# Kernel optimization log

Hardware: AMD Instinct MI355X
Metric: run time of the kernel (lower is better)

The kernel has to match this reference:

```python
import jax, jax.numpy as jnp
import numpy as np

B, N, K, LEN_INIT = 4, 4096, 10, 3
LEN_INPUT = 3 * (K + 1) + 3 * K + LEN_INIT  # 66


def setup_inputs() -> dict:
    key = jax.random.key(0)
    ks = jax.random.split(key, 6)
    return {
        "position": jax.random.normal(ks[0], (B, N, 3), dtype=jnp.float32),
        "velocity": jax.random.normal(ks[1], (B, N, 3), dtype=jnp.float32),
        "init_config": jax.random.normal(ks[2], (B, LEN_INIT), dtype=jnp.float32),
        "W1": jax.random.normal(ks[3], (32, LEN_INPUT), dtype=jnp.float32) * 0.1,
        "b1": jnp.zeros((32,), dtype=jnp.float32),
        "W2": jax.random.normal(ks[4], (16, 32), dtype=jnp.float32) * 0.1,
        "b2": jnp.zeros((16,), dtype=jnp.float32),
        "W3": jax.random.normal(ks[5], (6, 16), dtype=jnp.float32) * 0.1,
        "b3": jnp.zeros((6,), dtype=jnp.float32),
    }


def reference(position, velocity, init_config, W1, b1, W2, b2, W3, b3):
    Bc, Nc, _ = position.shape
    # pairwise squared distances [B,N,N]; same topk ordering as euclidean cdist
    sq = jnp.sum(position * position, axis=-1)  # [B,N]
    d2 = sq[:, :, None] + sq[:, None, :] - 2.0 * jnp.einsum("bnd,bmd->bnm", position, position)
    # k+1 nearest (including self), ascending distance
    _, nn_idx = jax.lax.top_k(-d2, K + 1)  # [B,N,K+1]
    # gather neighbor features per batch element
    vel_nn = jax.vmap(lambda v, i: v[i])(velocity, nn_idx)          # [B,N,K+1,3]
    pos_nn = jax.vmap(lambda p, i: p[i])(position, nn_idx[:, :, 1:])  # [B,N,K,3]
    pos_off = pos_nn - position[:, :, None, :]  # relative positions, no self
    feats = jnp.concatenate(
        [
            pos_off.reshape(Bc, Nc, 3 * K),
            vel_nn.reshape(Bc, Nc, 3 * (K + 1)),
            jnp.broadcast_to(init_config[:, None, :], (Bc, Nc, LEN_INIT)),
        ],
        axis=2,
    )  # [B,N,66]
    # three stacked linear layers (no nonlinearity, matching nn.Sequential of Linears)
    h = feats @ W1.T + b1
    h = h @ W2.T + b2
    pred = h @ W3.T + b3  # [B,N,6]
    return pred.at[:, :, :3].add(position)
```

## Files before the change

kernel.cpp:

```cpp
#include <hip/hip_runtime.h>
#include <stdint.h>

#define BATCH 4
#define NPTS 4096
#define KNN 11
#define LPQ 16
#define QPB 16
#define CHUNK 2048
#define NCHUNK (NPTS / CHUNK)
#define CPL (CHUNK / LPQ)

#define SENTINEL_BITS 0x433FFFFFFFFFFFFFll

__device__ __forceinline__ unsigned sortable_f32(float d) {
    unsigned b = __float_as_uint(d);
    unsigned m = (unsigned)(((int)b) >> 31) | 0x80000000u;
    return b ^ m;
}

__global__ __launch_bounds__(256, 4) void fused_kernel(
    const float* __restrict__ pos, const float* __restrict__ vel,
    const float* __restrict__ initc,
    const float* __restrict__ W1, const float* __restrict__ b1,
    const float* __restrict__ W2, const float* __restrict__ b2,
    const float* __restrict__ W3, const float* __restrict__ b3,
    float* __restrict__ out)
{
#pragma clang fp contract(off)
    __shared__ float4 sp[CHUNK + LPQ];

    int b    = blockIdx.x / (NPTS / QPB);
    int qblk = blockIdx.x % (NPTS / QPB);
    const float* pb = pos + (size_t)b * NPTS * 3;

    int q = threadIdx.x >> 4;
    int p = threadIdx.x & 15;
    int i = qblk * QPB + q;

    float xq = pb[3*i], yq = pb[3*i+1], zq = pb[3*i+2];
    float sqq = xq*xq + yq*yq + zq*zq;

    double kd[KNN];
#pragma unroll
    for (int k = 0; k < KNN; ++k) kd[k] = __longlong_as_double(SENTINEL_BITS);

    for (int c = 0; c < NCHUNK; ++c) {
        if (c) __syncthreads();
        for (int j = threadIdx.x; j < CHUNK; j += 256) {
            int g = c * CHUNK + j;
            float x = pb[3*g], y = pb[3*g+1], z = pb[3*g+2];
            float sq = x*x + y*y + z*z;
            sp[j + (j >> 7)] = make_float4(x, y, z, sq);
        }
        __syncthreads();

        int sbase = p * (CPL + 1);
        int jg    = c * CHUNK + p * CPL;
#pragma unroll 4
        for (int jl = 0; jl < CPL; ++jl) {
            float4 cc = sp[sbase + jl];
            float t = xq * cc.x;
            t = fmaf(yq, cc.y, t);
            t = fmaf(zq, cc.z, t);
            float d2 = (sqq + cc.w) - 2.0f * t;
            unsigned u = sortable_f32(d2);
            unsigned jj = (unsigned)(jg + jl);
            unsigned lo = (u << 12) | jj;
            unsigned hi = 0x43300000u | (u >> 20);
            double key = __longlong_as_double(
                ((long long)(int)hi << 32) | (unsigned long long)lo);
#pragma unroll
            for (int k = KNN-1; k > 0; --k) {
                double mn = fmin(kd[k], key);
                kd[k] = fmax(kd[k-1], mn);
            }
            kd[0] = fmin(kd[0], key);
        }
    }

    unsigned res[KNN];
#pragma unroll
    for (int r = 0; r < KNN; ++r) {
        double h = kd[0];
#pragma unroll
        for (int m = 1; m <= 8; m <<= 1)
            h = fmin(h, __shfl_xor(h, m, LPQ));
        long long hb = __double_as_longlong(h);
        res[r] = (unsigned)(hb & 0xFFF);
        bool own = (__double_as_longlong(kd[0]) == hb);
#pragma unroll
        for (int t = 0; t < KNN-1; ++t) kd[t] = own ? kd[t+1] : kd[t];
        kd[KNN-1] = own ? __longlong_as_double(SENTINEL_BITS) : kd[KNN-1];
    }

    const float* vb = vel + (size_t)b * NPTS * 3;

    const float* w0 = W1 + (2*p)   * 66;
    const float* w1 = W1 + (2*p+1) * 66;
    float a0 = b1[2*p], a1 = b1[2*p+1];
#pragma unroll
    for (int k = 1; k < KNN; ++k) {
        const float* pn = pb + 3*(int)res[k];
        float dx = pn[0] - xq, dy = pn[1] - yq, dz = pn[2] - zq;
        int ff = 3*(k-1);
        a0 = fmaf(dx, w0[ff+0], a0); a1 = fmaf(dx, w1[ff+0], a1);
        a0 = fmaf(dy, w0[ff+1], a0); a1 = fmaf(dy, w1[ff+1], a1);
        a0 = fmaf(dz, w0[ff+2], a0); a1 = fmaf(dz, w1[ff+2], a1);
    }
#pragma unroll
    for (int k = 0; k < KNN; ++k) {
        const float* vn = vb + 3*(int)res[k];
        int ff = 30 + 3*k;
        a0 = fmaf(vn[0], w0[ff+0], a0); a1 = fmaf(vn[0], w1[ff+0], a1);
        a0 = fmaf(vn[1], w0[ff+1], a0); a1 = fmaf(vn[1], w1[ff+1], a1);
        a0 = fmaf(vn[2], w0[ff+2], a0); a1 = fmaf(vn[2], w1[ff+2], a1);
    }
    float c0 = initc[b*3+0], c1 = initc[b*3+1], c2 = initc[b*3+2];
    a0 = fmaf(c0, w0[63], a0); a1 = fmaf(c0, w1[63], a1);
    a0 = fmaf(c1, w0[64], a0); a1 = fmaf(c1, w1[64], a1);
    a0 = fmaf(c2, w0[65], a0); a1 = fmaf(c2, w1[65], a1);

    float h2 = b2[p];
    const float* w2 = W2 + p * 32;
#pragma unroll
    for (int ii = 0; ii < 32; ++ii) {
        float h1v = __shfl((ii & 1) ? a1 : a0, ii >> 1, LPQ);
        h2 = fmaf(h1v, w2[ii], h2);
    }

    int o3 = p < 6 ? p : 0;
    float po = b3[o3];
    const float* w3 = W3 + o3 * 16;
#pragma unroll
    for (int ii = 0; ii < 16; ++ii) {
        float h2v = __shfl(h2, ii, LPQ);
        po = fmaf(h2v, w3[ii], po);
    }
    float resid = (p == 0) ? xq : (p == 1) ? yq : (p == 2) ? zq : 0.0f;
    po += resid;

    if (p < 6)
        out[((size_t)b * NPTS + (size_t)i) * 6 + p] = po;
}

extern "C" void kernel_launch(void* const* d_in, const int* in_sizes, int n_in,
                              void* d_out, int out_size, void* d_ws, size_t ws_size,
                              hipStream_t stream) {
    const float* pos   = (const float*)d_in[0];
    const float* vel   = (const float*)d_in[1];
    const float* initc = (const float*)d_in[2];
    const float* W1    = (const float*)d_in[3];
    const float* b1    = (const float*)d_in[4];
    const float* W2    = (const float*)d_in[5];
    const float* b2    = (const float*)d_in[6];
    const float* W3    = (const float*)d_in[7];
    const float* b3    = (const float*)d_in[8];
    float* out = (float*)d_out;

    fused_kernel<<<dim3(BATCH * (NPTS / QPB)), dim3(256), 0, stream>>>(
        pos, vel, initc, W1, b1, W2, b2, W3, b3, out);
}
```

Baseline: 143.7 us.

## Filter kNN candidates by group threshold and batch insertions via shared buffer

Adds a per-query distance threshold, taken as the 11th-best across the 16 lanes of a query, so that only candidates under it are written to a per-thread shared-memory buffer. The buffer is flushed into the register sorting network only when some lane fills it. This is meant to avoid running the 11-stage min/max insertion for every candidate. Chunk size is halved to make room for the buffer. The costs are extra LDS traffic, a wave-wide __any branch per iteration, periodic shuffle-based threshold refreshes, and the loop unroll dropping to 1.

Result: faster. 131.3 us (-8.6%).

```diff
diff --git a/kernel.cpp b/kernel.cpp
--- a/kernel.cpp
+++ b/kernel.cpp
@@ -6,11 +6,11 @@
 #define KNN 11
 #define LPQ 16
 #define QPB 16
-#define CHUNK 2048
+#define CHUNK 1024
 #define NCHUNK (NPTS / CHUNK)
 #define CPL (CHUNK / LPQ)
-
-#define SENTINEL_BITS 0x433FFFFFFFFFFFFFll
+#define BUFN 8
+#define SENT_BITS 0x433FFFFFFFFFFFFFll
 
 __device__ __forceinline__ unsigned sortable_f32(float d) {
     unsigned b = __float_as_uint(d);
@@ -28,13 +28,14 @@
 {
 #pragma clang fp contract(off)
     __shared__ float4 sp[CHUNK + LPQ];
-
-    int b    = blockIdx.x / (NPTS / QPB);
-    int qblk = blockIdx.x % (NPTS / QPB);
+    __shared__ unsigned long long buf[BUFN * 256];
+
+    int b    = blockIdx.x >> 8;
+    int qblk = blockIdx.x & 255;
+    int tid  = threadIdx.x;
     const float* pb = pos + (size_t)b * NPTS * 3;
 
-    int q = threadIdx.x >> 4;
-    int p = threadIdx.x & 15;
+    int q = tid >> 4, p = tid & 15;
     int i = qblk * QPB + q;
 
     float xq = pb[3*i], yq = pb[3*i+1], zq = pb[3*i+2];
@@ -42,21 +43,23 @@
 
     double kd[KNN];
 #pragma unroll
-    for (int k = 0; k < KNN; ++k) kd[k] = __longlong_as_double(SENTINEL_BITS);
+    for (int k = 0; k < KNN; ++k) kd[k] = __longlong_as_double(SENT_BITS);
+    unsigned tau_u = 0xFFFFFFFFu;
+    int cnt = 0;
 
     for (int c = 0; c < NCHUNK; ++c) {
         if (c) __syncthreads();
-        for (int j = threadIdx.x; j < CHUNK; j += 256) {
+        for (int j = tid; j < CHUNK; j += 256) {
             int g = c * CHUNK + j;
             float x = pb[3*g], y = pb[3*g+1], z = pb[3*g+2];
             float sq = x*x + y*y + z*z;
-            sp[j + (j >> 7)] = make_float4(x, y, z, sq);
+            sp[j + (j >> 6)] = make_float4(x, y, z, sq);
         }
         __syncthreads();
 
         int sbase = p * (CPL + 1);
         int jg    = c * CHUNK + p * CPL;
-#pragma unroll 4
+#pragma unroll 1
         for (int jl = 0; jl < CPL; ++jl) {
             float4 cc = sp[sbase + jl];
             float t = xq * cc.x;
@@ -64,18 +67,61 @@
             t = fmaf(zq, cc.z, t);
             float d2 = (sqq + cc.w) - 2.0f * t;
             unsigned u = sortable_f32(d2);
-            unsigned jj = (unsigned)(jg + jl);
-            unsigned lo = (u << 12) | jj;
-            unsigned hi = 0x43300000u | (u >> 20);
-            double key = __longlong_as_double(
-                ((long long)(int)hi << 32) | (unsigned long long)lo);
-#pragma unroll
-            for (int k = KNN-1; k > 0; --k) {
-                double mn = fmin(kd[k], key);
-                kd[k] = fmax(kd[k-1], mn);
+            if (u <= tau_u) {
+                unsigned jj = (unsigned)(jg + jl);
+                unsigned lo = (u << 12) | jj;
+                unsigned hi = 0x43300000u | (u >> 20);
+                buf[cnt * 256 + tid] =
+                    ((unsigned long long)hi << 32) | (unsigned long long)lo;
+                ++cnt;
             }
-            kd[0] = fmin(kd[0], key);
+            if (__any(cnt == BUFN)) {
+                for (int k = 0; k < BUFN; ++k) {
+                    unsigned long long kb = buf[k * 256 + tid];
+                    double key = (k < cnt) ? __longlong_as_double(kb)
+                                           : __longlong_as_double(SENT_BITS);
+#pragma unroll
+                    for (int kk = KNN-1; kk > 0; --kk) {
+                        double mn = fmin(kd[kk], key);
+                        kd[kk] = fmax(kd[kk-1], mn);
+                    }
+                    kd[0] = fmin(kd[0], key);
+                }
+                cnt = 0;
+                double tmp[KNN];
+#pragma unroll
+                for (int k = 0; k < KNN; ++k) tmp[k] = kd[k];
+                double h = tmp[0];
+#pragma unroll
+                for (int r = 0; r < KNN; ++r) {
+                    h = tmp[0];
+#pragma unroll
+                    for (int m = 1; m <= 8; m <<= 1)
+                        h = fmin(h, __shfl_xor(h, m, LPQ));
+                    bool own = (__double_as_longlong(tmp[0]) ==
+                                __double_as_longlong(h));
+#pragma unroll
+                    for (int t2 = 0; t2 < KNN-1; ++t2)
+                        tmp[t2] = own ? tmp[t2+1] : tmp[t2];
+                    tmp[KNN-1] = own ? __longlong_as_double(SENT_BITS)
+                                     : tmp[KNN-1];
+                }
+                tau_u = (unsigned)((unsigned long long)
+                                   __double_as_longlong(h) >> 12);
+            }
         }
+    }
+
+    for (int k = 0; k < BUFN; ++k) {
+        unsigned long long kb = buf[k * 256 + tid];
+        double key = (k < cnt) ? __longlong_as_double(kb)
+                               : __longlong_as_double(SENT_BITS);
+#pragma unroll
+        for (int kk = KNN-1; kk > 0; --kk) {
+            double mn = fmin(kd[kk], key);
+            kd[kk] = fmax(kd[kk-1], mn);
+        }
+        kd[0] = fmin(kd[0], key);
     }
 
     unsigned res[KNN];
@@ -90,7 +136,7 @@
         bool own = (__double_as_longlong(kd[0]) == hb);
 #pragma unroll
         for (int t = 0; t < KNN-1; ++t) kd[t] = own ? kd[t+1] : kd[t];
-        kd[KNN-1] = own ? __longlong_as_double(SENTINEL_BITS) : kd[KNN-1];
+        kd[KNN-1] = own ? __longlong_as_double(SENT_BITS) : kd[KNN-1];
     }
 
     const float* vb = vel + (size_t)b * NPTS * 3;
@@ -127,7 +173,6 @@
         float h1v = __shfl((ii & 1) ? a1 : a0, ii >> 1, LPQ);
         h2 = fmaf(h1v, w2[ii], h2);
     }
-
     int o3 = p < 6 ? p : 0;
     float po = b3[o3];
     const float* w3 = W3 + o3 * 16;
```
